# Kernel tuning notes

Measured on AMD Instinct MI355X. Metric: run time of the kernel, lower is better.

The kernel has to match this reference:

```python
import jax, jax.numpy as jnp
import numpy as np

ARITY = 2
GROUPS = 512
OUT_DIM = 16
ACT_INIT = 1.0
ACT_FACTOR = 1.0
BATCH = 8192


def setup_inputs() -> dict:
    key = jax.random.key(0)
    k1, k2 = jax.random.split(key)
    X = jax.random.normal(k1, (BATCH, GROUPS * ARITY), dtype=jnp.float32)
    # learned corner table: random signs scaled by act_init/act_factor, shape [G, 2^A, D]
    r = jax.random.randint(k2, (GROUPS, 2 ** ARITY, OUT_DIM), 0, 2)
    params = (r * 2 - 1).astype(jnp.float32) * (ACT_INIT / ACT_FACTOR)
    return {"X": X, "params": params}


def expand_params(params):
    # Binary corner table [G, 2^A, D] -> ternary grid [G, 3^A, D].
    # At step i, dim i (most-significant first) is expanded from {lo, hi}
    # to {lo, (lo+hi)/2, hi}, matching the torch view/stack loop.
    ep = params
    for i in range(ARITY):
        s0 = 3 ** i
        s1 = 2 ** (ARITY - i - 1)
        pv = ep.reshape(GROUPS, s0, 2, s1, OUT_DIM)
        lo, hi = pv[:, :, 0], pv[:, :, 1]
        ep = jnp.stack([lo, (lo + hi) * 0.5, hi], axis=2)
    return ep.reshape(GROUPS, 3 ** ARITY, OUT_DIM)


def reference(X, params):
    B = X.shape[0]
    X1 = X.reshape(B, GROUPS, ARITY)
    ep = expand_params(params)                      # [G, 3^A, D]
    # map inputs to grid coords: clamp to [-1,1], grid points at {0,1,2}
    t = jnp.clip(X1, -1.0, 1.0) + 1.0               # [B, G, A] in [0, 2]
    # per-dim linear hat weights over the 3 grid points: [B, G, A, 3]
    grid = jnp.arange(3, dtype=X.dtype)
    w = jnp.maximum(0.0, 1.0 - jnp.abs(t[..., None] - grid))
    # combine across arity dims (dim 0 = most significant base-3 digit)
    wk = w[:, :, 0, :]                              # [B, G, 3]
    for i in range(1, ARITY):
        wk = (wk[..., :, None] * w[:, :, i, None, :]).reshape(B, GROUPS, 3 ** (i + 1))
    # multilinear interpolation: [B,G,3^A] x [G,3^A,D] -> [B,G,D]
    out1 = jnp.einsum('bgk,gkd->bgd', wk, ep)
    return out1.reshape(B, GROUPS * OUT_DIM) * ACT_FACTOR
```

## Files before the change

kernel.cpp:

```cpp
#include <hip/hip_runtime.h>


#define BATCH   8192
#define GROUPS  512
#define OUT_DIM 16

__global__ __launch_bounds__(256) void corner_act_kernel(
    const float* __restrict__ X,
    const float* __restrict__ P,
    float* __restrict__ out)
{
    const int idx = blockIdx.x * 256 + threadIdx.x;
    const int q = idx & 3;
    const int g = (idx >> 2) & (GROUPS - 1);

    const float2 x = ((const float2*)X)[idx >> 2];
    const float a = (fminf(fmaxf(x.x, -1.0f), 1.0f) + 1.0f) * 0.5f;
    const float b = (fminf(fmaxf(x.y, -1.0f), 1.0f) + 1.0f) * 0.5f;

    const float w00 = (1.0f - a) * (1.0f - b);
    const float w01 = (1.0f - a) * b;
    const float w10 = a * (1.0f - b);
    const float w11 = a * b;

    const float4* p = (const float4*)(P + g * 64) + q;
    const float4 p0 = p[0];
    const float4 p1 = p[4];
    const float4 p2 = p[8];
    const float4 p3 = p[12];

    float4 o;
    o.x = w00 * p0.x + w01 * p1.x + w10 * p2.x + w11 * p3.x;
    o.y = w00 * p0.y + w01 * p1.y + w10 * p2.y + w11 * p3.y;
    o.z = w00 * p0.z + w01 * p1.z + w10 * p2.z + w11 * p3.z;
    o.w = w00 * p0.w + w01 * p1.w + w10 * p2.w + w11 * p3.w;

    ((float4*)out)[idx] = o;
}

extern "C" void kernel_launch(void* const* d_in, const int* in_sizes, int n_in,
                              void* d_out, int out_size, void* d_ws, size_t ws_size,
                              hipStream_t stream) {
    const float* X = (const float*)d_in[0];
    const float* P = (const float*)d_in[1];
    float* out = (float*)d_out;

    const int total_f4 = BATCH * GROUPS * (OUT_DIM / 4);
    const int block = 256;
    const int grid = total_f4 / block;
    corner_act_kernel<<<grid, block, 0, stream>>>(X, P, out);
}
```

Measured before the change: 328.4 us.

## Keep corner params in registers and loop over batch rows per thread

Each block now owns a 64-group chunk and a 32-row batch slice. Each thread loads its four parameter vectors once and reuses them across 32 batch rows instead of reloading them per output element. This cuts repeated parameter traffic and index math, which matters because the kernel is write-bandwidth bound. In exchange there are fewer threads (a 8x256 grid of 256-thread blocks) and some redundant X loads across the 4 lanes of each group.

Result: faster. 297.9 us (-9.3%).

```diff
diff --git a/kernel.cpp b/kernel.cpp
--- a/kernel.cpp
+++ b/kernel.cpp
@@ -4,38 +4,46 @@
 #define BATCH   8192
 #define GROUPS  512
 #define OUT_DIM 16
+#define GCHUNK  64
+#define BITER   32
+
+typedef float v4f __attribute__((ext_vector_type(4)));
+typedef float v2f __attribute__((ext_vector_type(2)));
 
 __global__ __launch_bounds__(256) void corner_act_kernel(
     const float* __restrict__ X,
     const float* __restrict__ P,
     float* __restrict__ out)
 {
-    const int idx = blockIdx.x * 256 + threadIdx.x;
-    const int q = idx & 3;
-    const int g = (idx >> 2) & (GROUPS - 1);
+    const int t  = threadIdx.x;
+    const int q  = t & 3;
+    const int g  = blockIdx.x * GCHUNK + (t >> 2);
 
-    const float2 x = ((const float2*)X)[idx >> 2];
-    const float a = (fminf(fmaxf(x.x, -1.0f), 1.0f) + 1.0f) * 0.5f;
-    const float b = (fminf(fmaxf(x.y, -1.0f), 1.0f) + 1.0f) * 0.5f;
+    const v4f* p = (const v4f*)P + g * 16 + q;
+    const v4f p0 = p[0];
+    const v4f p1 = p[4];
+    const v4f p2 = p[8];
+    const v4f p3 = p[12];
 
-    const float w00 = (1.0f - a) * (1.0f - b);
-    const float w01 = (1.0f - a) * b;
-    const float w10 = a * (1.0f - b);
-    const float w11 = a * b;
+    const v2f* __restrict__ Xv = (const v2f*)X + g;
+    v4f* __restrict__ Ov = (v4f*)out + blockIdx.x * 256 + t;
 
-    const float4* p = (const float4*)(P + g * 64) + q;
-    const float4 p0 = p[0];
-    const float4 p1 = p[4];
-    const float4 p2 = p[8];
-    const float4 p3 = p[12];
+    const int b0 = blockIdx.y * BITER;
 
-    float4 o;
-    o.x = w00 * p0.x + w01 * p1.x + w10 * p2.x + w11 * p3.x;
-    o.y = w00 * p0.y + w01 * p1.y + w10 * p2.y + w11 * p3.y;
-    o.z = w00 * p0.z + w01 * p1.z + w10 * p2.z + w11 * p3.z;
-    o.w = w00 * p0.w + w01 * p1.w + w10 * p2.w + w11 * p3.w;
+    #pragma unroll 4
+    for (int i = 0; i < BITER; ++i) {
+        const int b = b0 + i;
+        const v2f x = Xv[b * 512];
 
-    ((float4*)out)[idx] = o;
+        const float a  = (fminf(fmaxf(x.x, -1.0f), 1.0f) + 1.0f) * 0.5f;
+        const float bb = (fminf(fmaxf(x.y, -1.0f), 1.0f) + 1.0f) * 0.5f;
+        const float w00 = (1.0f - a) * (1.0f - bb);
+        const float w01 = (1.0f - a) * bb;
+        const float w10 = a * (1.0f - bb);
+        const float w11 = a * bb;
+
+        Ov[b * 2048] = w00 * p0 + w01 * p1 + w10 * p2 + w11 * p3;
+    }
 }
 
 extern "C" void kernel_launch(void* const* d_in, const int* in_sizes, int n_in,
@@ -45,8 +53,6 @@
     const float* P = (const float*)d_in[1];
     float* out = (float*)d_out;
 
-    const int total_f4 = BATCH * GROUPS * (OUT_DIM / 4);
-    const int block = 256;
-    const int grid = total_f4 / block;
-    corner_act_kernel<<<grid, block, 0, stream>>>(X, P, out);
+    dim3 grid(GROUPS / GCHUNK, BATCH / BITER);
+    corner_act_kernel<<<grid, dim3(256), 0, stream>>>(X, P, out);
 }
```
